# Kernel tuning notes

Measured on AMD Instinct MI355X. Metric: run time of the kernel, lower is better.

Reference implementation:

```python
import jax, jax.numpy as jnp
import numpy as np

N_NODES = 100000
N_EDGES = 3200000
NUM_FEATURES = 128
NUM_CLASSES = 32
H1, H2 = 64, 32


def _glorot(key, shape):
    lim = float(np.sqrt(6.0 / (shape[0] + shape[1])))
    return jax.random.uniform(key, shape, jnp.float32, -lim, lim)


def setup_inputs() -> dict:
    key = jax.random.key(0)
    ks = jax.random.split(key, 8)
    x = jax.random.normal(ks[0], (N_NODES, NUM_FEATURES), jnp.float32)
    edge_index = jax.random.randint(ks[1], (2, N_EDGES), 0, N_NODES, jnp.int64)
    return {
        "x": x,
        "edge_index": edge_index,
        "W1": _glorot(ks[2], (NUM_FEATURES, H1)), "b1": jnp.zeros((H1,), jnp.float32),
        "W2": _glorot(ks[3], (H1, H2)), "b2": jnp.zeros((H2,), jnp.float32),
        "Wf": _glorot(ks[4], (H2, H2)), "bf": jnp.zeros((H2,), jnp.float32),
        "Wo": _glorot(ks[5], (H2, NUM_CLASSES)), "bo": jnp.zeros((NUM_CLASSES,), jnp.float32),
    }


def gcn_conv(x, src, dst, n, W, b):
    # PyG GCNConv: add self-loops, symmetric normalization D^-1/2 A D^-1/2,
    # aggregate messages source -> target (dst = edge_index[1]).
    h = x @ W                                            # [N, F_out]
    deg = jax.ops.segment_sum(jnp.ones_like(dst, dtype=x.dtype), dst, num_segments=n)
    dinv = jnp.where(deg > 0, jax.lax.rsqrt(deg), 0.0)
    norm = dinv[src] * dinv[dst]                         # [E+N]
    msg = h[src] * norm[:, None]                         # gather + scale
    return jax.ops.segment_sum(msg, dst, num_segments=n) + b


def reference(x, edge_index, W1, b1, W2, b2, Wf, bf, Wo, bo):
    n = x.shape[0]
    loops = jnp.arange(n, dtype=edge_index.dtype)
    src = jnp.concatenate([edge_index[0], loops])
    dst = jnp.concatenate([edge_index[1], loops])
    h = jax.nn.relu(gcn_conv(x, src, dst, n, W1, b1))
    h = gcn_conv(h, src, dst, n, W2, b2)
    h = jax.nn.relu(h @ Wf + bf)
    return h @ Wo + bo
```

## Files before the change

### kernel.cpp

```cpp
#include <hip/hip_runtime.h>
#include <hip/hip_bf16.h>


#define N_NODES 100000
#define N_EDGES 3200000
#define F_IN    128
#define H1F     64
#define H2F     32
#define NCLS    32
#define SCAN_BLOCK 1024
#define SCAN_CHUNKS ((N_NODES + SCAN_BLOCK - 1) / SCAN_BLOCK)
#define NTIL2 (N_NODES / 32)
#define NCNT2 ((N_EDGES + 2048 - 1) / 2048)
#define NFRONT (NTIL2 + NCNT2)

typedef __attribute__((ext_vector_type(8))) short bf16x8;
typedef __attribute__((ext_vector_type(4))) float f32x4;

static __device__ __forceinline__ float b2f(__hip_bfloat16 v) {
    return __bfloat162float(v);
}
static __device__ __forceinline__ float us2f(unsigned short u) {
    return __uint_as_float(((unsigned)u) << 16);
}
static __device__ __forceinline__ unsigned short f2us(float f) {
    __hip_bfloat16 h = __float2bfloat16(f);
    return *(unsigned short*)&h;
}
static __device__ __forceinline__ float ld(const void* p, size_t i, int isbf) {
    return isbf ? b2f(((const __hip_bfloat16*)p)[i]) : ((const float*)p)[i];
}


__global__ void k_init(const void* xbuf, const void* eibuf, int* flags,
                       int* __restrict__ deg) {
    int t = blockIdx.x * blockDim.x + threadIdx.x;
    if (t < N_NODES) deg[t] = 0;
    if (blockIdx.x == 0 && threadIdx.x == 0) {
        const unsigned* ew = (const unsigned*)eibuf;
        int z = 0;
        for (int k = 0; k < 256; ++k) z += (ew[2 * k + 1] == 0u) ? 1 : 0;
        flags[0] = (z >= 200) ? 1 : 0;
        const unsigned* xw = (const unsigned*)xbuf;
        int inr = 0;
        for (int k = 0; k < 256; ++k) {
            unsigned fb = (xw[k] & 0xFFFFu) << 16;
            float a = fabsf(__uint_as_float(fb));
            inr += (a >= 1e-4f && a <= 20.0f) ? 1 : 0;
        }
        flags[1] = (inr >= 160) ? 1 : 0;
    }
}

__global__ void __launch_bounds__(256)
k_front(const void* __restrict__ x, const void* __restrict__ W1,
        const int* __restrict__ ei,
        int* __restrict__ deg, int* __restrict__ aux,
        unsigned short* __restrict__ h1, const int* __restrict__ flags) {
    int blk = blockIdx.x, tid = threadIdx.x;

    if (blk % 3 == 0) {
        int t = (blk / 3) * 256 + tid;
        int e0 = t * 8;
        if (e0 >= N_EDGES) return;
        int d[8];
        if (flags[0]) {
            const int4* p = (const int4*)(ei + 2 * (size_t)(N_EDGES + e0));
            int4 a = p[0], b = p[1], c = p[2], g = p[3];
            d[0] = a.x; d[1] = a.z; d[2] = b.x; d[3] = b.z;
            d[4] = c.x; d[5] = c.z; d[6] = g.x; d[7] = g.z;
        } else {
            const int4* p = (const int4*)(ei + (size_t)N_EDGES + e0);
            int4 a = p[0], b = p[1];
            d[0] = a.x; d[1] = a.y; d[2] = a.z; d[3] = a.w;
            d[4] = b.x; d[5] = b.y; d[6] = b.z; d[7] = b.w;
        }
        int r[8];
#pragma unroll
        for (int j = 0; j < 8; ++j)
            r[j] = ((unsigned)d[j] < N_NODES) ? atomicAdd(&deg[d[j]], 1) : 0;
        *(int4*)(aux + e0)     = make_int4(r[0], r[1], r[2], r[3]);
        *(int4*)(aux + e0 + 4) = make_int4(r[4], r[5], r[6], r[7]);
        return;
    }

    int tile = blk - blk / 3 - 1;
    int isbf = flags[1];
    int wave = __builtin_amdgcn_readfirstlane(tid >> 6);
    int lane = tid & 63;
    size_t nbase = (size_t)tile * 32 + (size_t)wave * 8;

    float acc[8];
#pragma unroll
    for (int i = 0; i < 8; ++i) acc[i] = 0.f;

    if (isbf) {
        const unsigned short* w  = (const unsigned short*)W1;
        const unsigned short* xp = (const unsigned short*)x;
#pragma unroll 4
        for (int k2 = 0; k2 < 64; ++k2) {
            float wa = us2f(w[(2 * k2) * H1F + lane]);
            float wb = us2f(w[(2 * k2 + 1) * H1F + lane]);
#pragma unroll
            for (int i = 0; i < 8; ++i) {
                float xa = us2f(xp[(nbase + i) * F_IN + 2 * k2]);
                float xb = us2f(xp[(nbase + i) * F_IN + 2 * k2 + 1]);
                acc[i] += xa * wa;
                acc[i] += xb * wb;
            }
        }
    } else {
        const float* w  = (const float*)W1;
        const float* xp = (const float*)x;
#pragma unroll 4
        for (int k2 = 0; k2 < 64; ++k2) {
            float wa = w[(2 * k2) * H1F + lane];
            float wb = w[(2 * k2 + 1) * H1F + lane];
#pragma unroll
            for (int i = 0; i < 8; ++i) {
                float xa = xp[(nbase + i) * F_IN + 2 * k2];
                float xb = xp[(nbase + i) * F_IN + 2 * k2 + 1];
                acc[i] += xa * wa;
                acc[i] += xb * wb;
            }
        }
    }

#pragma unroll
    for (int i = 0; i < 8; ++i)
        h1[(nbase + i) * H1F + lane] = f2us(acc[i]);
}

__global__ void k_scanA(const int* __restrict__ deg, int* __restrict__ partial,
                        float* __restrict__ dinv) {
    __shared__ int red[16];
    int b = blockIdx.x, t = threadIdx.x;
    int i = b * SCAN_BLOCK + t;
    int v = (i < N_NODES) ? deg[i] : 0;
    if (i < N_NODES) dinv[i] = rsqrtf((float)v + 1.0f);
    for (int off = 32; off; off >>= 1) v += __shfl_down(v, off, 64);
    if ((t & 63) == 0) red[t >> 6] = v;
    __syncthreads();
    if (t == 0) {
        int s = 0;
        for (int k = 0; k < 16; ++k) s += red[k];
        partial[b] = s;
    }
}

__global__ void k_scanC(const int* __restrict__ deg, const int* __restrict__ partial,
                        int* __restrict__ rowptr) {
    __shared__ int wsum[16];
    __shared__ int red[16];
    int b = blockIdx.x, t = threadIdx.x, lane = t & 63, w = t >> 6;
    int i = b * SCAN_BLOCK + t;
    int c = (t < SCAN_CHUNKS && t < b) ? partial[t] : 0;
    for (int off = 32; off; off >>= 1) c += __shfl_down(c, off, 64);
    if (lane == 0) red[w] = c;
    int v = (i < N_NODES) ? deg[i] : 0;
    for (int off = 1; off < 64; off <<= 1) {
        int u = __shfl_up(v, off, 64);
        if (lane >= off) v += u;
    }
    if (lane == 63) wsum[w] = v;
    __syncthreads();
    if (t == 0) {
        int run = 0;
        for (int k = 0; k < 16; ++k) { int s = wsum[k]; wsum[k] = run; run += s; }
        int sc = 0;
        for (int k = 0; k < 16; ++k) sc += red[k];
        red[0] = sc;
    }
    __syncthreads();
    int incl = v + wsum[w] + red[0];
    if (i < N_NODES) rowptr[i + 1] = incl;
    if (b == 0 && t == 0) rowptr[0] = 0;
}

__global__ void __launch_bounds__(256)
k_scatter(const int* __restrict__ ei, const int* __restrict__ aux,
          const int* __restrict__ rowptr, int* __restrict__ csr,
          const int* __restrict__ flags) {
    int t = blockIdx.x * blockDim.x + threadIdx.x;
    int e0 = t * 8;
    if (e0 >= N_EDGES) return;
    int s[8], d[8];
    if (flags[0]) {
        const int4* ps = (const int4*)(ei + 2 * (size_t)e0);
#pragma unroll
        for (int q = 0; q < 4; ++q) {
            int4 a = ps[q];
            s[2 * q] = a.x; s[2 * q + 1] = a.z;
        }
        const int4* pd = (const int4*)(ei + 2 * (size_t)(N_EDGES + e0));
#pragma unroll
        for (int q = 0; q < 4; ++q) {
            int4 c = pd[q];
            d[2 * q] = c.x; d[2 * q + 1] = c.z;
        }
    } else {
        const int4* ps = (const int4*)(ei + (size_t)e0);
#pragma unroll
        for (int q = 0; q < 2; ++q) {
            int4 a = ps[q];
            s[4 * q] = a.x; s[4 * q + 1] = a.y; s[4 * q + 2] = a.z; s[4 * q + 3] = a.w;
        }
        const int4* pd = (const int4*)(ei + (size_t)N_EDGES + e0);
#pragma unroll
        for (int q = 0; q < 2; ++q) {
            int4 c = pd[q];
            d[4 * q] = c.x; d[4 * q + 1] = c.y; d[4 * q + 2] = c.z; d[4 * q + 3] = c.w;
        }
    }
    int a8[8];
    {
        int4 av0 = *(const int4*)(aux + e0);
        int4 av1 = *(const int4*)(aux + e0 + 4);
        a8[0] = av0.x; a8[1] = av0.y; a8[2] = av0.z; a8[3] = av0.w;
        a8[4] = av1.x; a8[5] = av1.y; a8[6] = av1.z; a8[7] = av1.w;
    }
    int rp[8];
#pragma unroll
    for (int j = 0; j < 8; ++j) {
        bool ok = (unsigned)s[j] < N_NODES && (unsigned)d[j] < N_NODES;
        rp[j] = ok ? rowptr[d[j]] : -1;
    }
#pragma unroll
    for (int j = 0; j < 8; ++j) {
        if (rp[j] >= 0) csr[rp[j] + a8[j]] = s[j];
    }
}

__global__ void k_agg1gemm2(const unsigned short* __restrict__ h1,
                            const float* __restrict__ dinv,
                            const int* __restrict__ rowptr, const int* __restrict__ csr,
                            const void* __restrict__ b1, const void* __restrict__ W2,
                            unsigned short* __restrict__ h2, const int* __restrict__ flags) {
    int n    = (blockIdx.x * blockDim.x + threadIdx.x) >> 6;
    n = __builtin_amdgcn_readfirstlane(n);
    int lane = threadIdx.x & 63;
    if (n >= N_NODES) return;
    int beg = rowptr[n], end = rowptr[n + 1];
    float dn  = dinv[n];
    float acc = dn * us2f(h1[(size_t)n * H1F + lane]);
    int e = beg;
    int nfull = (end - beg) >> 3;
    if (nfull > 0) {
        int i0[8], i1[8];
        float w0[8]; unsigned short v0[8];
#pragma unroll
        for (int j = 0; j < 8; ++j) i0[j] = csr[e + j];
        if (nfull > 1) {
#pragma unroll
            for (int j = 0; j < 8; ++j) i1[j] = csr[e + 8 + j];
        }
#pragma unroll
        for (int j = 0; j < 8; ++j) {
            w0[j] = dinv[i0[j]];
            v0[j] = h1[(size_t)i0[j] * H1F + lane];
        }
        for (int b = 0; b < nfull; ++b) {
            int i2[8]; float w1[8]; unsigned short v1[8];
            if (b + 2 < nfull) {
#pragma unroll
                for (int j = 0; j < 8; ++j) i2[j] = csr[e + 16 + j];
            }
            if (b + 1 < nfull) {
#pragma unroll
                for (int j = 0; j < 8; ++j) {
                    w1[j] = dinv[i1[j]];
                    v1[j] = h1[(size_t)i1[j] * H1F + lane];
                }
            }
            acc += w0[0] * us2f(v0[0]); acc += w0[1] * us2f(v0[1]);
            acc += w0[2] * us2f(v0[2]); acc += w0[3] * us2f(v0[3]);
            acc += w0[4] * us2f(v0[4]); acc += w0[5] * us2f(v0[5]);
            acc += w0[6] * us2f(v0[6]); acc += w0[7] * us2f(v0[7]);
            e += 8;
#pragma unroll
            for (int j = 0; j < 8; ++j) { i1[j] = i2[j]; w0[j] = w1[j]; v0[j] = v1[j]; }
        }
    }
    for (; e + 3 < end; e += 4) {
        int s0 = csr[e], s1 = csr[e + 1], s2 = csr[e + 2], s3 = csr[e + 3];
        float w0 = dinv[s0], w1 = dinv[s1], w2 = dinv[s2], w3 = dinv[s3];
        unsigned short v0 = h1[(size_t)s0 * H1F + lane];
        unsigned short v1 = h1[(size_t)s1 * H1F + lane];
        unsigned short v2 = h1[(size_t)s2 * H1F + lane];
        unsigned short v3 = h1[(size_t)s3 * H1F + lane];
        acc += w0 * us2f(v0); acc += w1 * us2f(v1);
        acc += w2 * us2f(v2); acc += w3 * us2f(v3);
    }
    for (; e < end; ++e) {
        int s = csr[e];
        acc += dinv[s] * us2f(h1[(size_t)s * H1F + lane]);
    }
    acc *= dn;
    int isbf = flags[1];
    float bv = isbf ? b2f(((const __hip_bfloat16*)b1)[lane]) : ((const float*)b1)[lane];
    float v  = fmaxf(acc + bv, 0.f);
    int f = lane & 31, h = lane >> 5;
    float part = 0.f;
    if (isbf) {
        const __hip_bfloat16* w = (const __hip_bfloat16*)W2;
#pragma unroll
        for (int j = 0; j < 32; ++j) {
            int k = h * 32 + j;
            part += __shfl(v, k, 64) * b2f(w[k * H2F + f]);
        }
    } else {
        const float* w = (const float*)W2;
#pragma unroll
        for (int j = 0; j < 32; ++j) {
            int k = h * 32 + j;
            part += __shfl(v, k, 64) * w[k * H2F + f];
        }
    }
    part += __shfl(part, lane ^ 32, 64);
    if (h == 0) h2[(size_t)n * H2F + f] = f2us(part);
}

__global__ void GCN_51737176048479_kernel(const unsigned short* __restrict__ h2,
                                          const float* __restrict__ dinv,
                                          const int* __restrict__ rowptr,
                                          const int* __restrict__ csr,
                                          const void* __restrict__ b2v,
                                          const void* __restrict__ Wf,
                                          const void* __restrict__ bfv,
                                          const void* __restrict__ Wo,
                                          const void* __restrict__ bov,
                                          void* __restrict__ out,
                                          const int* __restrict__ flags) {
    int tid = blockIdx.x * blockDim.x + threadIdx.x;
    int n   = tid >> 5;
    int f   = threadIdx.x & 31;
    if (n >= N_NODES) return;
    int isbf = flags[1];
    int beg = rowptr[n], end = rowptr[n + 1];
    float dn = dinv[n];
    float ar = dn * us2f(h2[(size_t)n * H2F + f]);
    int e = beg;
    int nfull = (end - beg) >> 3;
    if (nfull > 0) {
        int i0[8], i1[8];
        float w0[8]; unsigned short v0[8];
#pragma unroll
        for (int j = 0; j < 8; ++j) i0[j] = csr[e + j];
        if (nfull > 1) {
#pragma unroll
            for (int j = 0; j < 8; ++j) i1[j] = csr[e + 8 + j];
        }
#pragma unroll
        for (int j = 0; j < 8; ++j) {
            w0[j] = dinv[i0[j]];
            v0[j] = h2[(size_t)i0[j] * H2F + f];
        }
        for (int b = 0; b < nfull; ++b) {
            int i2[8]; float w1[8]; unsigned short v1[8];
            if (b + 2 < nfull) {
#pragma unroll
                for (int j = 0; j < 8; ++j) i2[j] = csr[e + 16 + j];
            }
            if (b + 1 < nfull) {
#pragma unroll
                for (int j = 0; j < 8; ++j) {
                    w1[j] = dinv[i1[j]];
                    v1[j] = h2[(size_t)i1[j] * H2F + f];
                }
            }
            ar += w0[0] * us2f(v0[0]); ar += w0[1] * us2f(v0[1]);
            ar += w0[2] * us2f(v0[2]); ar += w0[3] * us2f(v0[3]);
            ar += w0[4] * us2f(v0[4]); ar += w0[5] * us2f(v0[5]);
            ar += w0[6] * us2f(v0[6]); ar += w0[7] * us2f(v0[7]);
            e += 8;
#pragma unroll
            for (int j = 0; j < 8; ++j) { i1[j] = i2[j]; w0[j] = w1[j]; v0[j] = v1[j]; }
        }
    }
    for (; e + 3 < end; e += 4) {
        int s0 = csr[e], s1 = csr[e + 1], s2 = csr[e + 2], s3 = csr[e + 3];
        float w0 = dinv[s0], w1 = dinv[s1], w2 = dinv[s2], w3 = dinv[s3];
        unsigned short v0 = h2[(size_t)s0 * H2F + f];
        unsigned short v1 = h2[(size_t)s1 * H2F + f];
        unsigned short v2 = h2[(size_t)s2 * H2F + f];
        unsigned short v3 = h2[(size_t)s3 * H2F + f];
        ar += w0 * us2f(v0); ar += w1 * us2f(v1);
        ar += w2 * us2f(v2); ar += w3 * us2f(v3);
    }
    for (; e < end; ++e) {
        int s = csr[e];
        ar += dinv[s] * us2f(h2[(size_t)s * H2F + f]);
    }
    ar = ar * dn + ld(b2v, f, isbf);
    float acc1 = 0.f;
#pragma unroll
    for (int k = 0; k < H2F; ++k)
        acc1 += __shfl(ar, k, 32) * ld(Wf, (size_t)k * H2F + f, isbf);
    float u = fmaxf(acc1 + ld(bfv, f, isbf), 0.f);
    float acc2 = 0.f;
#pragma unroll
    for (int k = 0; k < H2F; ++k)
        acc2 += __shfl(u, k, 32) * ld(Wo, (size_t)k * NCLS + f, isbf);
    float r = acc2 + ld(bov, f, isbf);
    size_t oi = (size_t)n * NCLS + f;
    if (isbf) ((__hip_bfloat16*)out)[oi] = __float2bfloat16(r);
    else      ((float*)out)[oi] = r;
}

extern "C" void kernel_launch(void* const* d_in, const int* in_sizes, int n_in,
                              void* d_out, int out_size, void* d_ws, size_t ws_size,
                              hipStream_t stream) {
    const void* x  = d_in[0];
    const int*  ei = (const int*)d_in[1];
    const void* W1 = d_in[2];
    const void* b1 = d_in[3];
    const void* W2 = d_in[4];
    const void* b2 = d_in[5];
    const void* Wf = d_in[6];
    const void* bf = d_in[7];
    const void* Wo = d_in[8];
    const void* bo = d_in[9];

    char* ws = (char*)d_ws;
    int*            deg      = (int*)  (ws + 0);
    int*            rowptr   = (int*)  (ws + (512u  << 10));
    float*          dinv     = (float*)(ws + (1024u << 10));
    int*            flags    = (int*)  (ws + (1434u << 10));
    int*            partial  = (int*)  (ws + (1444u << 10));
    int*            aux      = (int*)  (ws + (2u  << 20));
    int*            csr      = (int*)  (ws + (15u << 20));
    unsigned short* h1       = (unsigned short*)(ws + (28u << 20));
    unsigned short* h2       = (unsigned short*)(ws + (41u << 20));

    const int B = 256;

    k_init<<<SCAN_CHUNKS, SCAN_BLOCK, 0, stream>>>(x, ei, flags, deg);

    k_front<<<NFRONT, B, 0, stream>>>(x, W1, ei, deg, aux, h1, flags);

    k_scanA<<<SCAN_CHUNKS, SCAN_BLOCK, 0, stream>>>(deg, partial, dinv);
    k_scanC<<<SCAN_CHUNKS, SCAN_BLOCK, 0, stream>>>(deg, partial, rowptr);
    k_scatter<<<(N_EDGES / 8 + B - 1) / B, B, 0, stream>>>(ei, aux, rowptr, csr, flags);

    k_agg1gemm2<<<(N_NODES * 64 + B - 1) / B, B, 0, stream>>>(h1, dinv, rowptr, csr,
                                                              b1, W2, h2, flags);
    GCN_51737176048479_kernel<<<(N_NODES * 32 + B - 1) / B, B, 0, stream>>>(
        h2, dinv, rowptr, csr, b2, Wf, bf, Wo, bo, d_out, flags);
}
```

Before: 504.0 us.

## Gather two bf16 features per lane in both aggregation kernels

Both the layer-1 aggregation and the final aggregation kernel now load packed 32-bit words holding two bf16 features per lane. This halves the threads per node (32 lanes for 64 features, 16 lanes for 32 features) and halves the number of gather instructions and the redundant csr/dinv loads per node. The software-pipelined prefetch loop is replaced with a plain 8-wide unrolled loop. The dense epilogues are rewritten to shuffle two values per lane, and the output is stored as packed pairs. The change trades memory-level parallelism per node for fewer load instructions and index reads.

```diff
diff --git a/kernel.cpp b/kernel.cpp
--- a/kernel.cpp
+++ b/kernel.cpp
@@ -22,6 +22,12 @@
 }
 static __device__ __forceinline__ float us2f(unsigned short u) {
     return __uint_as_float(((unsigned)u) << 16);
+}
+static __device__ __forceinline__ float lo2f(unsigned u) {
+    return __uint_as_float((u & 0xFFFFu) << 16);
+}
+static __device__ __forceinline__ float hi2f(unsigned u) {
+    return __uint_as_float(u & 0xFFFF0000u);
 }
 static __device__ __forceinline__ unsigned short f2us(float f) {
     __hip_bfloat16 h = __float2bfloat16(f);
@@ -231,180 +237,197 @@
     }
 }
 
-__global__ void k_agg1gemm2(const unsigned short* __restrict__ h1,
-                            const float* __restrict__ dinv,
-                            const int* __restrict__ rowptr, const int* __restrict__ csr,
-                            const void* __restrict__ b1, const void* __restrict__ W2,
-                            unsigned short* __restrict__ h2, const int* __restrict__ flags) {
-    int n    = (blockIdx.x * blockDim.x + threadIdx.x) >> 6;
-    n = __builtin_amdgcn_readfirstlane(n);
-    int lane = threadIdx.x & 63;
+__global__ void __launch_bounds__(256)
+k_agg1gemm2(const unsigned short* __restrict__ h1,
+            const float* __restrict__ dinv,
+            const int* __restrict__ rowptr, const int* __restrict__ csr,
+            const void* __restrict__ b1, const void* __restrict__ W2,
+            unsigned short* __restrict__ h2, const int* __restrict__ flags) {
+    int tid = blockIdx.x * blockDim.x + threadIdx.x;
+    int n = tid >> 5;
+    int g = threadIdx.x & 31;
     if (n >= N_NODES) return;
     int beg = rowptr[n], end = rowptr[n + 1];
-    float dn  = dinv[n];
-    float acc = dn * us2f(h1[(size_t)n * H1F + lane]);
+    float dn = dinv[n];
+    const unsigned* h1w = (const unsigned*)h1;
+    unsigned su = h1w[(size_t)n * 32 + g];
+    float ax = dn * lo2f(su);
+    float ay = dn * hi2f(su);
     int e = beg;
-    int nfull = (end - beg) >> 3;
-    if (nfull > 0) {
-        int i0[8], i1[8];
-        float w0[8]; unsigned short v0[8];
-#pragma unroll
-        for (int j = 0; j < 8; ++j) i0[j] = csr[e + j];
-        if (nfull > 1) {
-#pragma unroll
-            for (int j = 0; j < 8; ++j) i1[j] = csr[e + 8 + j];
-        }
-#pragma unroll
-        for (int j = 0; j < 8; ++j) {
-            w0[j] = dinv[i0[j]];
-            v0[j] = h1[(size_t)i0[j] * H1F + lane];
-        }
-        for (int b = 0; b < nfull; ++b) {
-            int i2[8]; float w1[8]; unsigned short v1[8];
-            if (b + 2 < nfull) {
-#pragma unroll
-                for (int j = 0; j < 8; ++j) i2[j] = csr[e + 16 + j];
-            }
-            if (b + 1 < nfull) {
-#pragma unroll
-                for (int j = 0; j < 8; ++j) {
-                    w1[j] = dinv[i1[j]];
-                    v1[j] = h1[(size_t)i1[j] * H1F + lane];
-                }
-            }
-            acc += w0[0] * us2f(v0[0]); acc += w0[1] * us2f(v0[1]);
-            acc += w0[2] * us2f(v0[2]); acc += w0[3] * us2f(v0[3]);
-            acc += w0[4] * us2f(v0[4]); acc += w0[5] * us2f(v0[5]);
-            acc += w0[6] * us2f(v0[6]); acc += w0[7] * us2f(v0[7]);
-            e += 8;
-#pragma unroll
-            for (int j = 0; j < 8; ++j) { i1[j] = i2[j]; w0[j] = w1[j]; v0[j] = v1[j]; }
-        }
+    for (; e + 7 < end; e += 8) {
+        int s0 = csr[e],     s1 = csr[e + 1], s2 = csr[e + 2], s3 = csr[e + 3];
+        int s4 = csr[e + 4], s5 = csr[e + 5], s6 = csr[e + 6], s7 = csr[e + 7];
+        float w0 = dinv[s0], w1 = dinv[s1], w2 = dinv[s2], w3 = dinv[s3];
+        float w4 = dinv[s4], w5 = dinv[s5], w6 = dinv[s6], w7 = dinv[s7];
+        unsigned u0 = h1w[(size_t)s0 * 32 + g];
+        unsigned u1 = h1w[(size_t)s1 * 32 + g];
+        unsigned u2 = h1w[(size_t)s2 * 32 + g];
+        unsigned u3 = h1w[(size_t)s3 * 32 + g];
+        unsigned u4 = h1w[(size_t)s4 * 32 + g];
+        unsigned u5 = h1w[(size_t)s5 * 32 + g];
+        unsigned u6 = h1w[(size_t)s6 * 32 + g];
+        unsigned u7 = h1w[(size_t)s7 * 32 + g];
+        ax += w0 * lo2f(u0); ay += w0 * hi2f(u0);
+        ax += w1 * lo2f(u1); ay += w1 * hi2f(u1);
+        ax += w2 * lo2f(u2); ay += w2 * hi2f(u2);
+        ax += w3 * lo2f(u3); ay += w3 * hi2f(u3);
+        ax += w4 * lo2f(u4); ay += w4 * hi2f(u4);
+        ax += w5 * lo2f(u5); ay += w5 * hi2f(u5);
+        ax += w6 * lo2f(u6); ay += w6 * hi2f(u6);
+        ax += w7 * lo2f(u7); ay += w7 * hi2f(u7);
     }
     for (; e + 3 < end; e += 4) {
         int s0 = csr[e], s1 = csr[e + 1], s2 = csr[e + 2], s3 = csr[e + 3];
         float w0 = dinv[s0], w1 = dinv[s1], w2 = dinv[s2], w3 = dinv[s3];
-        unsigned short v0 = h1[(size_t)s0 * H1F + lane];
-        unsigned short v1 = h1[(size_t)s1 * H1F + lane];
-        unsigned short v2 = h1[(size_t)s2 * H1F + lane];
-        unsigned short v3 = h1[(size_t)s3 * H1F + lane];
-        acc += w0 * us2f(v0); acc += w1 * us2f(v1);
-        acc += w2 * us2f(v2); acc += w3 * us2f(v3);
+        unsigned u0 = h1w[(size_t)s0 * 32 + g];
+        unsigned u1 = h1w[(size_t)s1 * 32 + g];
+        unsigned u2 = h1w[(size_t)s2 * 32 + g];
+        unsigned u3 = h1w[(size_t)s3 * 32 + g];
+        ax += w0 * lo2f(u0); ay += w0 * hi2f(u0);
+        ax += w1 * lo2f(u1); ay += w1 * hi2f(u1);
+        ax += w2 * lo2f(u2); ay += w2 * hi2f(u2);
+        ax += w3 * lo2f(u3); ay += w3 * hi2f(u3);
     }
     for (; e < end; ++e) {
         int s = csr[e];
-        acc += dinv[s] * us2f(h1[(size_t)s * H1F + lane]);
-    }
-    acc *= dn;
+        float w = dinv[s];
+        unsigned u = h1w[(size_t)s * 32 + g];
+        ax += w * lo2f(u); ay += w * hi2f(u);
+    }
+    ax *= dn; ay *= dn;
     int isbf = flags[1];
-    float bv = isbf ? b2f(((const __hip_bfloat16*)b1)[lane]) : ((const float*)b1)[lane];
-    float v  = fmaxf(acc + bv, 0.f);
-    int f = lane & 31, h = lane >> 5;
-    float part = 0.f;
+    float vx = fmaxf(ax + ld(b1, 2 * g, isbf), 0.f);
+    float vy = fmaxf(ay + ld(b1, 2 * g + 1, isbf), 0.f);
+    float p0 = 0.f, p1 = 0.f;
     if (isbf) {
         const __hip_bfloat16* w = (const __hip_bfloat16*)W2;
 #pragma unroll
-        for (int j = 0; j < 32; ++j) {
-            int k = h * 32 + j;
-            part += __shfl(v, k, 64) * b2f(w[k * H2F + f]);
+        for (int j = 0; j < 16; ++j) {
+            p0 += __shfl(vx, j, 32) * b2f(w[(2 * j) * H2F + g]);
+            p0 += __shfl(vy, j, 32) * b2f(w[(2 * j + 1) * H2F + g]);
+        }
+#pragma unroll
+        for (int j = 16; j < 32; ++j) {
+            p1 += __shfl(vx, j, 32) * b2f(w[(2 * j) * H2F + g]);
+            p1 += __shfl(vy, j, 32) * b2f(w[(2 * j + 1) * H2F + g]);
         }
     } else {
         const float* w = (const float*)W2;
 #pragma unroll
-        for (int j = 0; j < 32; ++j) {
-            int k = h * 32 + j;
-            part += __shfl(v, k, 64) * w[k * H2F + f];
-        }
-    }
-    part += __shfl(part, lane ^ 32, 64);
-    if (h == 0) h2[(size_t)n * H2F + f] = f2us(part);
-}
-
-__global__ void GCN_51737176048479_kernel(const unsigned short* __restrict__ h2,
-                                          const float* __restrict__ dinv,
-                                          const int* __restrict__ rowptr,
-                                          const int* __restrict__ csr,
-                                          const void* __restrict__ b2v,
-                                          const void* __restrict__ Wf,
-                                          const void* __restrict__ bfv,
-                                          const void* __restrict__ Wo,
-                                          const void* __restrict__ bov,
-                                          void* __restrict__ out,
-                                          const int* __restrict__ flags) {
+        for (int j = 0; j < 16; ++j) {
+            p0 += __shfl(vx, j, 32) * w[(2 * j) * H2F + g];
+            p0 += __shfl(vy, j, 32) * w[(2 * j + 1) * H2F + g];
+        }
+#pragma unroll
+        for (int j = 16; j < 32; ++j) {
+            p1 += __shfl(vx, j, 32) * w[(2 * j) * H2F + g];
+            p1 += __shfl(vy, j, 32) * w[(2 * j + 1) * H2F + g];
+        }
+    }
+    h2[(size_t)n * H2F + g] = f2us(p0 + p1);
+}
+
+__global__ void __launch_bounds__(256)
+GCN_51737176048479_kernel(const unsigned short* __restrict__ h2,
+                          const float* __restrict__ dinv,
+                          const int* __restrict__ rowptr,
+                          const int* __restrict__ csr,
+                          const void* __restrict__ b2v,
+                          const void* __restrict__ Wf,
+                          const void* __restrict__ bfv,
+                          const void* __restrict__ Wo,
+                          const void* __restrict__ bov,
+                          void* __restrict__ out,
+                          const int* __restrict__ flags) {
     int tid = blockIdx.x * blockDim.x + threadIdx.x;
-    int n   = tid >> 5;
-    int f   = threadIdx.x & 31;
+    int n = tid >> 4;
+    int g = threadIdx.x & 15;
     if (n >= N_NODES) return;
     int isbf = flags[1];
     int beg = rowptr[n], end = rowptr[n + 1];
     float dn = dinv[n];
-    float ar = dn * us2f(h2[(size_t)n * H2F + f]);
+    const unsigned* h2w = (const unsigned*)h2;
+    unsigned su = h2w[(size_t)n * 16 + g];
+    float ax = dn * lo2f(su);
+    float ay = dn * hi2f(su);
     int e = beg;
-    int nfull = (end - beg) >> 3;
-    if (nfull > 0) {
-        int i0[8], i1[8];
-        float w0[8]; unsigned short v0[8];
-#pragma unroll
-        for (int j = 0; j < 8; ++j) i0[j] = csr[e + j];
-        if (nfull > 1) {
-#pragma unroll
-            for (int j = 0; j < 8; ++j) i1[j] = csr[e + 8 + j];
-        }
-#pragma unroll
-        for (int j = 0; j < 8; ++j) {
-            w0[j] = dinv[i0[j]];
-            v0[j] = h2[(size_t)i0[j] * H2F + f];
-        }
-        for (int b = 0; b < nfull; ++b) {
-            int i2[8]; float w1[8]; unsigned short v1[8];
-            if (b + 2 < nfull) {
-#pragma unroll
-                for (int j = 0; j < 8; ++j) i2[j] = csr[e + 16 + j];
-            }
-            if (b + 1 < nfull) {
-#pragma unroll
-                for (int j = 0; j < 8; ++j) {
-                    w1[j] = dinv[i1[j]];
-                    v1[j] = h2[(size_t)i1[j] * H2F + f];
-                }
-            }
-            ar += w0[0] * us2f(v0[0]); ar += w0[1] * us2f(v0[1]);
-            ar += w0[2] * us2f(v0[2]); ar += w0[3] * us2f(v0[3]);
-            ar += w0[4] * us2f(v0[4]); ar += w0[5] * us2f(v0[5]);
-            ar += w0[6] * us2f(v0[6]); ar += w0[7] * us2f(v0[7]);
-            e += 8;
-#pragma unroll
-            for (int j = 0; j < 8; ++j) { i1[j] = i2[j]; w0[j] = w1[j]; v0[j] = v1[j]; }
-        }
+    for (; e + 7 < end; e += 8) {
+        int s0 = csr[e],     s1 = csr[e + 1], s2 = csr[e + 2], s3 = csr[e + 3];
+        int s4 = csr[e + 4], s5 = csr[e + 5], s6 = csr[e + 6], s7 = csr[e + 7];
+        float w0 = dinv[s0], w1 = dinv[s1], w2 = dinv[s2], w3 = dinv[s3];
+        float w4 = dinv[s4], w5 = dinv[s5], w6 = dinv[s6], w7 = dinv[s7];
+        unsigned u0 = h2w[(size_t)s0 * 16 + g];
+        unsigned u1 = h2w[(size_t)s1 * 16 + g];
+        unsigned u2 = h2w[(size_t)s2 * 16 + g];
+        unsigned u3 = h2w[(size_t)s3 * 16 + g];
+        unsigned u4 = h2w[(size_t)s4 * 16 + g];
+        unsigned u5 = h2w[(size_t)s5 * 16 + g];
+        unsigned u6 = h2w[(size_t)s6 * 16 + g];
+        unsigned u7 = h2w[(size_t)s7 * 16 + g];
+        ax += w0 * lo2f(u0); ay += w0 * hi2f(u0);
+        ax += w1 * lo2f(u1); ay += w1 * hi2f(u1);
+        ax += w2 * lo2f(u2); ay += w2 * hi2f(u2);
+        ax += w3 * lo2f(u3); ay += w3 * hi2f(u3);
+        ax += w4 * lo2f(u4); ay += w4 * hi2f(u4);
+        ax += w5 * lo2f(u5); ay += w5 * hi2f(u5);
+        ax += w6 * lo2f(u6); ay += w6 * hi2f(u6);
+        ax += w7 * lo2f(u7); ay += w7 * hi2f(u7);
     }
     for (; e + 3 < end; e += 4) {
         int s0 = csr[e], s1 = csr[e + 1], s2 = csr[e + 2], s3 = csr[e + 3];
         float w0 = dinv[s0], w1 = dinv[s1], w2 = dinv[s2], w3 = dinv[s3];
-        unsigned short v0 = h2[(size_t)s0 * H2F + f];
-        unsigned short v1 = h2[(size_t)s1 * H2F + f];
-        unsigned short v2 = h2[(size_t)s2 * H2F + f];
-        unsigned short v3 = h2[(size_t)s3 * H2F + f];
-        ar += w0 * us2f(v0); ar += w1 * us2f(v1);
-        ar += w2 * us2f(v2); ar += w3 * us2f(v3);
+        unsigned u0 = h2w[(size_t)s0 * 16 + g];
+        unsigned u1 = h2w[(size_t)s1 * 16 + g];
+        unsigned u2 = h2w[(size_t)s2 * 16 + g];
+        unsigned u3 = h2w[(size_t)s3 * 16 + g];
+        ax += w0 * lo2f(u0); ay += w0 * hi2f(u0);
+        ax += w1 * lo2f(u1); ay += w1 * hi2f(u1);
+        ax += w2 * lo2f(u2); ay += w2 * hi2f(u2);
+        ax += w3 * lo2f(u3); ay += w3 * hi2f(u3);
     }
     for (; e < end; ++e) {
         int s = csr[e];
-        ar += dinv[s] * us2f(h2[(size_t)s * H2F + f]);
-    }
-    ar = ar * dn + ld(b2v, f, isbf);
-    float acc1 = 0.f;
-#pragma unroll
-    for (int k = 0; k < H2F; ++k)
-        acc1 += __shfl(ar, k, 32) * ld(Wf, (size_t)k * H2F + f, isbf);
-    float u = fmaxf(acc1 + ld(bfv, f, isbf), 0.f);
-    float acc2 = 0.f;
-#pragma unroll
-    for (int k = 0; k < H2F; ++k)
-        acc2 += __shfl(u, k, 32) * ld(Wo, (size_t)k * NCLS + f, isbf);
-    float r = acc2 + ld(bov, f, isbf);
-    size_t oi = (size_t)n * NCLS + f;
-    if (isbf) ((__hip_bfloat16*)out)[oi] = __float2bfloat16(r);
-    else      ((float*)out)[oi] = r;
+        float w = dinv[s];
+        unsigned u = h2w[(size_t)s * 16 + g];
+        ax += w * lo2f(u); ay += w * hi2f(u);
+    }
+    ax = ax * dn + ld(b2v, 2 * g, isbf);
+    ay = ay * dn + ld(b2v, 2 * g + 1, isbf);
+    float a1x = 0.f, a1y = 0.f;
+#pragma unroll
+    for (int j = 0; j < 16; ++j) {
+        float fx = __shfl(ax, j, 16);
+        float fy = __shfl(ay, j, 16);
+        float wx0 = ld(Wf, (size_t)(2 * j) * H2F + 2 * g, isbf);
+        float wx1 = ld(Wf, (size_t)(2 * j + 1) * H2F + 2 * g, isbf);
+        float wy0 = ld(Wf, (size_t)(2 * j) * H2F + 2 * g + 1, isbf);
+        float wy1 = ld(Wf, (size_t)(2 * j + 1) * H2F + 2 * g + 1, isbf);
+        a1x += fx * wx0; a1x += fy * wx1;
+        a1y += fx * wy0; a1y += fy * wy1;
+    }
+    float ux = fmaxf(a1x + ld(bfv, 2 * g, isbf), 0.f);
+    float uy = fmaxf(a1y + ld(bfv, 2 * g + 1, isbf), 0.f);
+    float a2x = 0.f, a2y = 0.f;
+#pragma unroll
+    for (int j = 0; j < 16; ++j) {
+        float fx = __shfl(ux, j, 16);
+        float fy = __shfl(uy, j, 16);
+        float wx0 = ld(Wo, (size_t)(2 * j) * NCLS + 2 * g, isbf);
+        float wx1 = ld(Wo, (size_t)(2 * j + 1) * NCLS + 2 * g, isbf);
+        float wy0 = ld(Wo, (size_t)(2 * j) * NCLS + 2 * g + 1, isbf);
+        float wy1 = ld(Wo, (size_t)(2 * j + 1) * NCLS + 2 * g + 1, isbf);
+        a2x += fx * wx0; a2x += fy * wx1;
+        a2y += fx * wy0; a2y += fy * wy1;
+    }
+    float rx = a2x + ld(bov, 2 * g, isbf);
+    float ry = a2y + ld(bov, 2 * g + 1, isbf);
+    if (isbf) {
+        unsigned pack = (unsigned)f2us(rx) | ((unsigned)f2us(ry) << 16);
+        ((unsigned*)out)[(size_t)n * 16 + g] = pack;
+    } else {
+        float2 r2 = make_float2(rx, ry);
+        ((float2*)out)[(size_t)n * 16 + g] = r2;
+    }
 }
 
 extern "C" void kernel_launch(void* const* d_in, const int* in_sizes, int n_in,
@@ -442,8 +465,8 @@
     k_scanC<<<SCAN_CHUNKS, SCAN_BLOCK, 0, stream>>>(deg, partial, rowptr);
     k_scatter<<<(N_EDGES / 8 + B - 1) / B, B, 0, stream>>>(ei, aux, rowptr, csr, flags);
 
-    k_agg1gemm2<<<(N_NODES * 64 + B - 1) / B, B, 0, stream>>>(h1, dinv, rowptr, csr,
+    k_agg1gemm2<<<(N_NODES * 32 + B - 1) / B, B, 0, stream>>>(h1, dinv, rowptr, csr,
                                                               b1, W2, h2, flags);
-    GCN_51737176048479_kernel<<<(N_NODES * 32 + B - 1) / B, B, 0, stream>>>(
+    GCN_51737176048479_kernel<<<(N_NODES * 16 + B - 1) / B, B, 0, stream>>>(
         h2, dinv, rowptr, csr, b2, Wf, bf, Wo, bo, d_out, flags);
 }
```

New measurement: 529.9 us. +5.1%, slower.

## Precompute per-edge source dinv in CSR order and simplify aggregation loops

Applied to the files above, without the earlier changes.

The scatter kernel now writes each edge's source dinv value into a CSR-ordered array next to the column index. Both aggregation kernels then read that weight with coalesced loads instead of gathering dinv[src] at random addresses. The software-pipelined 8-wide prefetch loop is replaced with a plain 8-wide unrolled loop. The cost is an extra random gather and 12.8MB write in scatter, a workspace-size condition that moves h1/h2, and more streamed bytes during aggregation.

```diff
diff --git a/kernel.cpp b/kernel.cpp
--- a/kernel.cpp
+++ b/kernel.cpp
@@ -179,7 +179,8 @@
 
 __global__ void __launch_bounds__(256)
 k_scatter(const int* __restrict__ ei, const int* __restrict__ aux,
-          const int* __restrict__ rowptr, int* __restrict__ csr,
+          const int* __restrict__ rowptr, const float* __restrict__ dinv,
+          int* __restrict__ csr, float* __restrict__ dinvE,
           const int* __restrict__ flags) {
     int t = blockIdx.x * blockDim.x + threadIdx.x;
     int e0 = t * 8;
@@ -225,14 +226,29 @@
         bool ok = (unsigned)s[j] < N_NODES && (unsigned)d[j] < N_NODES;
         rp[j] = ok ? rowptr[d[j]] : -1;
     }
-#pragma unroll
-    for (int j = 0; j < 8; ++j) {
-        if (rp[j] >= 0) csr[rp[j] + a8[j]] = s[j];
+    if (dinvE) {
+        float dv[8];
+#pragma unroll
+        for (int j = 0; j < 8; ++j) dv[j] = (rp[j] >= 0) ? dinv[s[j]] : 0.f;
+#pragma unroll
+        for (int j = 0; j < 8; ++j) {
+            if (rp[j] >= 0) {
+                int pos = rp[j] + a8[j];
+                csr[pos]   = s[j];
+                dinvE[pos] = dv[j];
+            }
+        }
+    } else {
+#pragma unroll
+        for (int j = 0; j < 8; ++j) {
+            if (rp[j] >= 0) csr[rp[j] + a8[j]] = s[j];
+        }
     }
 }
 
 __global__ void k_agg1gemm2(const unsigned short* __restrict__ h1,
                             const float* __restrict__ dinv,
+                            const float* __restrict__ dE,
                             const int* __restrict__ rowptr, const int* __restrict__ csr,
                             const void* __restrict__ b1, const void* __restrict__ W2,
                             unsigned short* __restrict__ h2, const int* __restrict__ flags) {
@@ -244,56 +260,52 @@
     float dn  = dinv[n];
     float acc = dn * us2f(h1[(size_t)n * H1F + lane]);
     int e = beg;
-    int nfull = (end - beg) >> 3;
-    if (nfull > 0) {
-        int i0[8], i1[8];
-        float w0[8]; unsigned short v0[8];
-#pragma unroll
-        for (int j = 0; j < 8; ++j) i0[j] = csr[e + j];
-        if (nfull > 1) {
-#pragma unroll
-            for (int j = 0; j < 8; ++j) i1[j] = csr[e + 8 + j];
-        }
-#pragma unroll
-        for (int j = 0; j < 8; ++j) {
-            w0[j] = dinv[i0[j]];
-            v0[j] = h1[(size_t)i0[j] * H1F + lane];
-        }
-        for (int b = 0; b < nfull; ++b) {
-            int i2[8]; float w1[8]; unsigned short v1[8];
-            if (b + 2 < nfull) {
-#pragma unroll
-                for (int j = 0; j < 8; ++j) i2[j] = csr[e + 16 + j];
-            }
-            if (b + 1 < nfull) {
-#pragma unroll
-                for (int j = 0; j < 8; ++j) {
-                    w1[j] = dinv[i1[j]];
-                    v1[j] = h1[(size_t)i1[j] * H1F + lane];
-                }
-            }
-            acc += w0[0] * us2f(v0[0]); acc += w0[1] * us2f(v0[1]);
-            acc += w0[2] * us2f(v0[2]); acc += w0[3] * us2f(v0[3]);
-            acc += w0[4] * us2f(v0[4]); acc += w0[5] * us2f(v0[5]);
-            acc += w0[6] * us2f(v0[6]); acc += w0[7] * us2f(v0[7]);
-            e += 8;
-#pragma unroll
-            for (int j = 0; j < 8; ++j) { i1[j] = i2[j]; w0[j] = w1[j]; v0[j] = v1[j]; }
-        }
-    }
-    for (; e + 3 < end; e += 4) {
-        int s0 = csr[e], s1 = csr[e + 1], s2 = csr[e + 2], s3 = csr[e + 3];
-        float w0 = dinv[s0], w1 = dinv[s1], w2 = dinv[s2], w3 = dinv[s3];
-        unsigned short v0 = h1[(size_t)s0 * H1F + lane];
-        unsigned short v1 = h1[(size_t)s1 * H1F + lane];
-        unsigned short v2 = h1[(size_t)s2 * H1F + lane];
-        unsigned short v3 = h1[(size_t)s3 * H1F + lane];
-        acc += w0 * us2f(v0); acc += w1 * us2f(v1);
-        acc += w2 * us2f(v2); acc += w3 * us2f(v3);
-    }
-    for (; e < end; ++e) {
-        int s = csr[e];
-        acc += dinv[s] * us2f(h1[(size_t)s * H1F + lane]);
+    if (dE) {
+        for (; e + 7 < end; e += 8) {
+            int s0 = csr[e],     s1 = csr[e + 1], s2 = csr[e + 2], s3 = csr[e + 3];
+            int s4 = csr[e + 4], s5 = csr[e + 5], s6 = csr[e + 6], s7 = csr[e + 7];
+            float w0 = dE[e],     w1 = dE[e + 1], w2 = dE[e + 2], w3 = dE[e + 3];
+            float w4 = dE[e + 4], w5 = dE[e + 5], w6 = dE[e + 6], w7 = dE[e + 7];
+            unsigned short v0 = h1[(size_t)s0 * H1F + lane];
+            unsigned short v1 = h1[(size_t)s1 * H1F + lane];
+            unsigned short v2 = h1[(size_t)s2 * H1F + lane];
+            unsigned short v3 = h1[(size_t)s3 * H1F + lane];
+            unsigned short v4 = h1[(size_t)s4 * H1F + lane];
+            unsigned short v5 = h1[(size_t)s5 * H1F + lane];
+            unsigned short v6 = h1[(size_t)s6 * H1F + lane];
+            unsigned short v7 = h1[(size_t)s7 * H1F + lane];
+            acc += w0 * us2f(v0); acc += w1 * us2f(v1);
+            acc += w2 * us2f(v2); acc += w3 * us2f(v3);
+            acc += w4 * us2f(v4); acc += w5 * us2f(v5);
+            acc += w6 * us2f(v6); acc += w7 * us2f(v7);
+        }
+        for (; e < end; ++e) {
+            int s = csr[e];
+            acc += dE[e] * us2f(h1[(size_t)s * H1F + lane]);
+        }
+    } else {
+        for (; e + 7 < end; e += 8) {
+            int s0 = csr[e],     s1 = csr[e + 1], s2 = csr[e + 2], s3 = csr[e + 3];
+            int s4 = csr[e + 4], s5 = csr[e + 5], s6 = csr[e + 6], s7 = csr[e + 7];
+            float w0 = dinv[s0], w1 = dinv[s1], w2 = dinv[s2], w3 = dinv[s3];
+            float w4 = dinv[s4], w5 = dinv[s5], w6 = dinv[s6], w7 = dinv[s7];
+            unsigned short v0 = h1[(size_t)s0 * H1F + lane];
+            unsigned short v1 = h1[(size_t)s1 * H1F + lane];
+            unsigned short v2 = h1[(size_t)s2 * H1F + lane];
+            unsigned short v3 = h1[(size_t)s3 * H1F + lane];
+            unsigned short v4 = h1[(size_t)s4 * H1F + lane];
+            unsigned short v5 = h1[(size_t)s5 * H1F + lane];
+            unsigned short v6 = h1[(size_t)s6 * H1F + lane];
+            unsigned short v7 = h1[(size_t)s7 * H1F + lane];
+            acc += w0 * us2f(v0); acc += w1 * us2f(v1);
+            acc += w2 * us2f(v2); acc += w3 * us2f(v3);
+            acc += w4 * us2f(v4); acc += w5 * us2f(v5);
+            acc += w6 * us2f(v6); acc += w7 * us2f(v7);
+        }
+        for (; e < end; ++e) {
+            int s = csr[e];
+            acc += dinv[s] * us2f(h1[(size_t)s * H1F + lane]);
+        }
     }
     acc *= dn;
     int isbf = flags[1];
@@ -322,6 +334,7 @@
 
 __global__ void GCN_51737176048479_kernel(const unsigned short* __restrict__ h2,
                                           const float* __restrict__ dinv,
+                                          const float* __restrict__ dE,
                                           const int* __restrict__ rowptr,
                                           const int* __restrict__ csr,
                                           const void* __restrict__ b2v,
@@ -340,56 +353,52 @@
     float dn = dinv[n];
     float ar = dn * us2f(h2[(size_t)n * H2F + f]);
     int e = beg;
-    int nfull = (end - beg) >> 3;
-    if (nfull > 0) {
-        int i0[8], i1[8];
-        float w0[8]; unsigned short v0[8];
-#pragma unroll
-        for (int j = 0; j < 8; ++j) i0[j] = csr[e + j];
-        if (nfull > 1) {
-#pragma unroll
-            for (int j = 0; j < 8; ++j) i1[j] = csr[e + 8 + j];
-        }
-#pragma unroll
-        for (int j = 0; j < 8; ++j) {
-            w0[j] = dinv[i0[j]];
-            v0[j] = h2[(size_t)i0[j] * H2F + f];
-        }
-        for (int b = 0; b < nfull; ++b) {
-            int i2[8]; float w1[8]; unsigned short v1[8];
-            if (b + 2 < nfull) {
-#pragma unroll
-                for (int j = 0; j < 8; ++j) i2[j] = csr[e + 16 + j];
-            }
-            if (b + 1 < nfull) {
-#pragma unroll
-                for (int j = 0; j < 8; ++j) {
-                    w1[j] = dinv[i1[j]];
-                    v1[j] = h2[(size_t)i1[j] * H2F + f];
-                }
-            }
-            ar += w0[0] * us2f(v0[0]); ar += w0[1] * us2f(v0[1]);
-            ar += w0[2] * us2f(v0[2]); ar += w0[3] * us2f(v0[3]);
-            ar += w0[4] * us2f(v0[4]); ar += w0[5] * us2f(v0[5]);
-            ar += w0[6] * us2f(v0[6]); ar += w0[7] * us2f(v0[7]);
-            e += 8;
-#pragma unroll
-            for (int j = 0; j < 8; ++j) { i1[j] = i2[j]; w0[j] = w1[j]; v0[j] = v1[j]; }
-        }
-    }
-    for (; e + 3 < end; e += 4) {
-        int s0 = csr[e], s1 = csr[e + 1], s2 = csr[e + 2], s3 = csr[e + 3];
-        float w0 = dinv[s0], w1 = dinv[s1], w2 = dinv[s2], w3 = dinv[s3];
-        unsigned short v0 = h2[(size_t)s0 * H2F + f];
-        unsigned short v1 = h2[(size_t)s1 * H2F + f];
-        unsigned short v2 = h2[(size_t)s2 * H2F + f];
-        unsigned short v3 = h2[(size_t)s3 * H2F + f];
-        ar += w0 * us2f(v0); ar += w1 * us2f(v1);
-        ar += w2 * us2f(v2); ar += w3 * us2f(v3);
-    }
-    for (; e < end; ++e) {
-        int s = csr[e];
-        ar += dinv[s] * us2f(h2[(size_t)s * H2F + f]);
+    if (dE) {
+        for (; e + 7 < end; e += 8) {
+            int s0 = csr[e],     s1 = csr[e + 1], s2 = csr[e + 2], s3 = csr[e + 3];
+            int s4 = csr[e + 4], s5 = csr[e + 5], s6 = csr[e + 6], s7 = csr[e + 7];
+            float w0 = dE[e],     w1 = dE[e + 1], w2 = dE[e + 2], w3 = dE[e + 3];
+            float w4 = dE[e + 4], w5 = dE[e + 5], w6 = dE[e + 6], w7 = dE[e + 7];
+            unsigned short v0 = h2[(size_t)s0 * H2F + f];
+            unsigned short v1 = h2[(size_t)s1 * H2F + f];
+            unsigned short v2 = h2[(size_t)s2 * H2F + f];
+            unsigned short v3 = h2[(size_t)s3 * H2F + f];
+            unsigned short v4 = h2[(size_t)s4 * H2F + f];
+            unsigned short v5 = h2[(size_t)s5 * H2F + f];
+            unsigned short v6 = h2[(size_t)s6 * H2F + f];
+            unsigned short v7 = h2[(size_t)s7 * H2F + f];
+            ar += w0 * us2f(v0); ar += w1 * us2f(v1);
+            ar += w2 * us2f(v2); ar += w3 * us2f(v3);
+            ar += w4 * us2f(v4); ar += w5 * us2f(v5);
+            ar += w6 * us2f(v6); ar += w7 * us2f(v7);
+        }
+        for (; e < end; ++e) {
+            int s = csr[e];
+            ar += dE[e] * us2f(h2[(size_t)s * H2F + f]);
+        }
+    } else {
+        for (; e + 7 < end; e += 8) {
+            int s0 = csr[e],     s1 = csr[e + 1], s2 = csr[e + 2], s3 = csr[e + 3];
+            int s4 = csr[e + 4], s5 = csr[e + 5], s6 = csr[e + 6], s7 = csr[e + 7];
+            float w0 = dinv[s0], w1 = dinv[s1], w2 = dinv[s2], w3 = dinv[s3];
+            float w4 = dinv[s4], w5 = dinv[s5], w6 = dinv[s6], w7 = dinv[s7];
+            unsigned short v0 = h2[(size_t)s0 * H2F + f];
+            unsigned short v1 = h2[(size_t)s1 * H2F + f];
+            unsigned short v2 = h2[(size_t)s2 * H2F + f];
+            unsigned short v3 = h2[(size_t)s3 * H2F + f];
+            unsigned short v4 = h2[(size_t)s4 * H2F + f];
+            unsigned short v5 = h2[(size_t)s5 * H2F + f];
+            unsigned short v6 = h2[(size_t)s6 * H2F + f];
+            unsigned short v7 = h2[(size_t)s7 * H2F + f];
+            ar += w0 * us2f(v0); ar += w1 * us2f(v1);
+            ar += w2 * us2f(v2); ar += w3 * us2f(v3);
+            ar += w4 * us2f(v4); ar += w5 * us2f(v5);
+            ar += w6 * us2f(v6); ar += w7 * us2f(v7);
+        }
+        for (; e < end; ++e) {
+            int s = csr[e];
+            ar += dinv[s] * us2f(h2[(size_t)s * H2F + f]);
+        }
     }
     ar = ar * dn + ld(b2v, f, isbf);
     float acc1 = 0.f;
@@ -429,8 +438,10 @@
     int*            partial  = (int*)  (ws + (1444u << 10));
     int*            aux      = (int*)  (ws + (2u  << 20));
     int*            csr      = (int*)  (ws + (15u << 20));
-    unsigned short* h1       = (unsigned short*)(ws + (28u << 20));
-    unsigned short* h2       = (unsigned short*)(ws + (41u << 20));
+    int use_de = (ws_size >= (61ull << 20)) ? 1 : 0;
+    float*          dinvE    = use_de ? (float*)(ws + (28u << 20)) : (float*)0;
+    unsigned short* h1       = (unsigned short*)(ws + ((use_de ? 41u : 28u) << 20));
+    unsigned short* h2       = (unsigned short*)(ws + ((use_de ? 54u : 41u) << 20));
 
     const int B = 256;
 
@@ -440,10 +451,11 @@
 
     k_scanA<<<SCAN_CHUNKS, SCAN_BLOCK, 0, stream>>>(deg, partial, dinv);
     k_scanC<<<SCAN_CHUNKS, SCAN_BLOCK, 0, stream>>>(deg, partial, rowptr);
-    k_scatter<<<(N_EDGES / 8 + B - 1) / B, B, 0, stream>>>(ei, aux, rowptr, csr, flags);
-
-    k_agg1gemm2<<<(N_NODES * 64 + B - 1) / B, B, 0, stream>>>(h1, dinv, rowptr, csr,
-                                                              b1, W2, h2, flags);
+    k_scatter<<<(N_EDGES / 8 + B - 1) / B, B, 0, stream>>>(ei, aux, rowptr, dinv,
+                                                           csr, dinvE, flags);
+
+    k_agg1gemm2<<<(N_NODES * 64 + B - 1) / B, B, 0, stream>>>(h1, dinv, dinvE, rowptr,
+                                                              csr, b1, W2, h2, flags);
     GCN_51737176048479_kernel<<<(N_NODES * 32 + B - 1) / B, B, 0, stream>>>(
-        h2, dinv, rowptr, csr, b2, Wf, bf, Wo, bo, d_out, flags);
-}
+        h2, dinv, dinvE, rowptr, csr, b2, Wf, bf, Wo, bo, d_out, flags);
+}
```

Measured after the change: 554.0 us. 9.9% more time.
